# Kernel tuning notes

Measured on AMD Instinct MI355X. Metric: run time of the kernel, lower is better.

Reference implementation:

```python
import jax, jax.numpy as jnp
import numpy as np
from jax import lax

B, DIM, HEADS, H, W = 8, 384, 8, 64, 64
HEAD_C = DIM // HEADS        # 48 -> topk k's: 24, 32, 36, 38
HID = int(DIM * 2.66)        # 1021
EPS_LN = 1e-5
EPS_N = 1e-12
SMALL = 1e-6


def conv2d(x, w, b, pad, groups=1):
    out = lax.conv_general_dilated(
        x, w, (1, 1), [(pad, pad), (pad, pad)],
        feature_group_count=groups,
        dimension_numbers=('NCHW', 'OIHW', 'NCHW'))
    return out + b[None, :, None, None]


def l2n(x):
    # torch F.normalize(dim=-1): x / max(||x||_2, eps)
    n = jnp.linalg.norm(x, axis=-1, keepdims=True)
    return x / jnp.maximum(n, EPS_N)


def layer_norm_c(x, w, b):
    # WithBias LayerNorm over channel dim (module does to_3d -> LN(c) -> to_4d)
    xt = jnp.transpose(x, (0, 2, 3, 1))  # b h w c
    mu = xt.mean(-1, keepdims=True)
    var = xt.var(-1, keepdims=True)      # unbiased=False
    y = (xt - mu) / jnp.sqrt(var + EPS_LN) * w + b
    return jnp.transpose(y, (0, 3, 1, 2))


def setup_inputs() -> dict:
    key = jax.random.key(0)
    ks = iter(jax.random.split(key, 40))
    rn = lambda shape, s=0.02: jax.random.normal(next(ks), shape, jnp.float32) * s
    return dict(
        x=jax.random.normal(next(ks), (B, DIM, H, W), jnp.float32),
        spf=jax.random.normal(next(ks), (1, 3, H, W), jnp.float32),
        ln1_w=jnp.ones((DIM,)), ln1_b=jnp.zeros((DIM,)),
        qkv_w=rn((3 * DIM, DIM, 1, 1)), qkv_b=jnp.zeros((3 * DIM,)),
        qkvdw_w=rn((3 * DIM, 1, 3, 3)), qkvdw_b=jnp.zeros((3 * DIM,)),
        proj_w=rn((DIM, 3, 3, 3)), proj_b=jnp.zeros((DIM,)),
        temperature=jnp.ones((HEADS, 1, 1)),
        a1=jnp.array([0.2]), a2=jnp.array([0.2]),
        a3=jnp.array([0.2]), a4=jnp.array([0.2]),
        wmix=jnp.ones((2,)),
        pout_w=rn((DIM, DIM, 1, 1)), pout_b=jnp.zeros((DIM,)),
        ln2_w=jnp.ones((DIM,)), ln2_b=jnp.zeros((DIM,)),
        pin_w=rn((2 * HID, DIM, 1, 1)), pin_b=jnp.zeros((2 * HID,)),
        dw_w=rn((HID, 1, 3, 3)), dw_b=jnp.zeros((HID,)),
        lin_w=rn((HID, HID)), lin_b=jnp.zeros((HID,)),
        adj_w=rn((HID, 2 * HID, 1, 1)), adj_b=jnp.zeros((HID,)),
        fout_w=rn((DIM, HID, 1, 1)), fout_b=jnp.zeros((DIM,)),
    )


def reference(x, spf, ln1_w, ln1_b, qkv_w, qkv_b, qkvdw_w, qkvdw_b,
              proj_w, proj_b, temperature, a1, a2, a3, a4, wmix,
              pout_w, pout_b, ln2_w, ln2_b, pin_w, pin_b, dw_w, dw_b,
              lin_w, lin_b, adj_w, adj_b, fout_w, fout_b):
    # ---------- Attention ----------
    xn = layer_norm_c(x, ln1_w, ln1_b)
    qkv = conv2d(conv2d(xn, qkv_w, qkv_b, 0), qkvdw_w, qkvdw_b, 1, groups=3 * DIM)
    q, k, v = jnp.split(qkv, 3, axis=1)
    q1 = l2n(q)                               # normalize along W axis
    spm = conv2d(jnp.broadcast_to(l2n(spf), (B, 3, H, W)), proj_w, proj_b, 1)
    qs = l2n((q1 * spm).reshape(B, HEADS, HEAD_C, H * W))
    kr = l2n(k.reshape(B, HEADS, HEAD_C, H * W))
    vr = v.reshape(B, HEADS, HEAD_C, H * W)
    attn = jnp.einsum('bhcn,bhdn->bhcd', qs, kr) * temperature[None]

    def masked_sm(kk):
        thr = lax.top_k(attn, kk)[0][..., -1:]  # k-th largest per row
        return jax.nn.softmax(jnp.where(attn >= thr, attn, attn * SMALL), axis=-1)

    attn0 = jax.nn.relu(attn)
    wsm = jax.nn.softmax(wmix)
    topks = [HEAD_C // 2, 2 * HEAD_C // 3, 3 * HEAD_C // 4, 4 * HEAD_C // 5]
    out = jnp.zeros((B, HEADS, HEAD_C, H * W), attn.dtype)
    for kk, c in zip(topks, [a1, a2, a3, a4]):
        blend = attn0 * wsm[0] + masked_sm(kk) * wsm[1]
        out = out + c * jnp.einsum('bhcd,bhdn->bhcn', blend, vr)
    out = out.reshape(B, DIM, H, W)
    x = x + conv2d(out, pout_w, pout_b, 0)

    # ---------- FeedForward ----------
    xn2 = layer_norm_c(x, ln2_w, ln2_b)
    p = conv2d(xn2, pin_w, pin_b, 0)
    x1, x2 = jnp.split(p, 2, axis=1)
    x1d = conv2d(x1, dw_w, dw_b, 1, groups=HID)
    x2l = jnp.einsum('bchw,oc->bohw', x2, lin_w) + lin_b[None, :, None, None]
    cat = jnp.concatenate([x1d, x2l], axis=1)    # [B, 2*HID, H, W]
    y1 = conv2d(cat, adj_w, adj_b, 0)
    y2 = y1  # second cat is identical under the intended (non-buggy) reading
    f = jax.nn.gelu(y1, approximate=False) * y2
    return x + conv2d(f, fout_w, fout_b, 0)
```

## Files before the change

### kernel.cpp

```cpp
#include <hip/hip_runtime.h>
#include <math.h>

typedef long long i64;
typedef unsigned short u16;
typedef unsigned int u32;

#define DIMC 384
#define DIM3 1152
#define HC 48
#define HWN 4096

using bf16x8 = __attribute__((ext_vector_type(8))) short;
using f32x4 = __attribute__((ext_vector_type(4))) float;

__device__ __forceinline__ float bf2f(u16 u) { u32 x = ((u32)u) << 16; return __uint_as_float(x); }
__device__ __forceinline__ u16 f2bf(float f) {
  u32 u = __float_as_uint(f);
  u32 r = u + 0x7FFFu + ((u >> 16) & 1u);
  return (u16)(r >> 16);
}
__device__ __forceinline__ u16 to_bf16(float f) { return f2bf(f); }
__device__ __forceinline__ u16 to_bf16(u16 u) { return u; }
__device__ __forceinline__ float ld_as_f(const float* p) { return *p; }
__device__ __forceinline__ float ld_as_f(const u16* p) { return bf2f(*p); }

__device__ __forceinline__ void gld_lds16(const u16* g, u16* l) {
  __builtin_amdgcn_global_load_lds(
      (const __attribute__((address_space(1))) void*)g,
      (__attribute__((address_space(3))) void*)l, 16, 0, 0);
}


__global__ void zero_kernel(float* __restrict__ p, int n) {
  int i = blockIdx.x * 256 + threadIdx.x;
  if (i < n) p[i] = 0.f;
}

__global__ void cvt_pad_kernel(const float* __restrict__ src, int lds, int M, int K,
                               u16* __restrict__ out) {
  int idx = blockIdx.x * 256 + threadIdx.x;
  int r = idx >> 10, k = idx & 1023;
  out[idx] = (r < M && k < K) ? f2bf(src[(i64)r * lds + k]) : (u16)0;
}

template <typename T>
__global__ void stats_kernel(const T* __restrict__ x, float* __restrict__ mu,
                             float* __restrict__ rs, int npix4) {
  int idx = blockIdx.x * 256 + threadIdx.x;
  if (idx >= npix4) return;
  int pg = idx * 4;
  int b = pg >> 12, p = pg & 4095;
  const T* xp = x + ((i64)b * DIMC) * HWN + p;
  float s0 = 0.f, s1 = 0.f, s2 = 0.f, s3 = 0.f;
  float q0 = 0.f, q1 = 0.f, q2 = 0.f, q3 = 0.f;
  for (int c = 0; c < DIMC; ++c) {
    const T* rp = xp + (i64)c * HWN;
    float v0 = ld_as_f(rp), v1 = ld_as_f(rp + 1), v2 = ld_as_f(rp + 2), v3 = ld_as_f(rp + 3);
    s0 += v0; s1 += v1; s2 += v2; s3 += v3;
    q0 += v0 * v0; q1 += v1 * v1; q2 += v2 * v2; q3 += v3 * v3;
  }
  const float inv = 1.f / DIMC;
  float4 m = make_float4(s0 * inv, s1 * inv, s2 * inv, s3 * inv);
  float4 r;
  r.x = rsqrtf(q0 * inv - m.x * m.x + 1e-5f);
  r.y = rsqrtf(q1 * inv - m.y * m.y + 1e-5f);
  r.z = rsqrtf(q2 * inv - m.z * m.z + 1e-5f);
  r.w = rsqrtf(q3 * inv - m.w * m.w + 1e-5f);
  *(float4*)(mu + (i64)pg) = m;
  *(float4*)(rs + (i64)pg) = r;
}

template <typename T>
__global__ __launch_bounds__(256) void ln_t_kernel(
    const T* __restrict__ x, const float* __restrict__ mu, const float* __restrict__ rs,
    const float* __restrict__ g, const float* __restrict__ bb, u16* __restrict__ y) {
  __shared__ u16 tile[64][66];
  int p0 = blockIdx.x * 64, c0 = blockIdx.y * 64, b = blockIdx.z;
  int t = threadIdx.x;
  int tp = t & 63, tq = t >> 6;
  float m = mu[b * 4096 + p0 + tp], r = rs[b * 4096 + p0 + tp];
  const T* xp = x + (i64)b * DIMC * HWN + (i64)c0 * 4096 + p0;
#pragma unroll
  for (int i = 0; i < 16; ++i) {
    int c = tq + i * 4;
    float v = ld_as_f(xp + (i64)c * 4096 + tp);
    tile[c][tp] = f2bf((v - m) * r * g[c0 + c] + bb[c0 + c]);
  }
  __syncthreads();
#pragma unroll
  for (int i = 0; i < 16; ++i) {
    int p = tq + i * 4;
    y[((i64)b * 4096 + p0 + p) * 384 + c0 + tp] = tile[tp][p];
  }
}

__global__ __launch_bounds__(256) void dw8_kernel(const u16* __restrict__ in, int ldin,
                                                  const float* __restrict__ w,
                                                  const float* __restrict__ bias,
                                                  u16* __restrict__ out, int ldo, int CH) {
  int t = threadIdx.x;
  int g = t & 31;
  int s = t >> 5;
  int c0 = (blockIdx.y * 32 + g) * 4;
  if (c0 >= ldo) return;
  i64 p0 = (i64)blockIdx.x * 32 + s * 4;
  i64 pb = p0 & ~4095LL;
  int sp = (int)(p0 & 4095);
  int y = sp >> 6, x0 = sp & 63;
  float wv[9][4];
  float acc[4][4];
#pragma unroll
  for (int cc = 0; cc < 4; ++cc) {
    bool val = (c0 + cc) < CH;
    float bv = val ? bias[c0 + cc] : 0.f;
#pragma unroll
    for (int i = 0; i < 4; ++i) acc[i][cc] = bv;
#pragma unroll
    for (int j = 0; j < 9; ++j) wv[j][cc] = val ? w[(c0 + cc) * 9 + j] : 0.f;
  }
#pragma unroll
  for (int dy = 0; dy < 3; ++dy) {
    int yy = y - 1 + dy;
    if ((unsigned)yy >= 64u) continue;
    float row[6][4];
#pragma unroll
    for (int dx = 0; dx < 6; ++dx) {
      int xx = x0 - 1 + dx;
      if ((unsigned)xx < 64u) {
        ushort4 v = *(const ushort4*)(in + (pb + yy * 64 + xx) * ldin + c0);
        row[dx][0] = bf2f(v.x); row[dx][1] = bf2f(v.y);
        row[dx][2] = bf2f(v.z); row[dx][3] = bf2f(v.w);
      } else {
        row[dx][0] = 0.f; row[dx][1] = 0.f; row[dx][2] = 0.f; row[dx][3] = 0.f;
      }
    }
#pragma unroll
    for (int i = 0; i < 4; ++i)
#pragma unroll
      for (int dx = 0; dx < 3; ++dx)
#pragma unroll
        for (int cc = 0; cc < 4; ++cc)
          acc[i][cc] += row[i + dx][cc] * wv[dy * 3 + dx][cc];
  }
#pragma unroll
  for (int i = 0; i < 4; ++i) {
    ushort4 o;
    o.x = (c0 + 0 < CH) ? f2bf(acc[i][0]) : (u16)0;
    o.y = (c0 + 1 < CH) ? f2bf(acc[i][1]) : (u16)0;
    o.z = (c0 + 2 < CH) ? f2bf(acc[i][2]) : (u16)0;
    o.w = (c0 + 3 < CH) ? f2bf(acc[i][3]) : (u16)0;
    *(ushort4*)(out + (p0 + i) * ldo + c0) = o;
  }
}

__global__ __launch_bounds__(192) void dwqnorm_kernel(
    const u16* __restrict__ qkv, const float* __restrict__ w9,
    const float* __restrict__ bias, const float* __restrict__ spm,
    const u16* __restrict__ kv, u16* __restrict__ QS,
    float* __restrict__ qssq, float* __restrict__ kssq) {
  int y = blockIdx.x;
  int b = blockIdx.y;
  int c = blockIdx.z * 192 + threadIdx.x;
  float wv[9];
#pragma unroll
  for (int j = 0; j < 9; ++j) wv[j] = w9[c * 9 + j];
  float bv = bias[c];
  float acc[64];
#pragma unroll
  for (int i = 0; i < 64; ++i) acc[i] = bv;
  i64 rowbase = (i64)b * 4096;
#pragma unroll
  for (int dy = 0; dy < 3; ++dy) {
    int yy = y - 1 + dy;
    if ((unsigned)yy >= 64u) continue;
    const u16* rp = qkv + (rowbase + yy * 64) * 1152 + c;
    float w0 = wv[dy * 3 + 0], w1 = wv[dy * 3 + 1], w2 = wv[dy * 3 + 2];
#pragma unroll
    for (int xi = 0; xi < 64; ++xi) {
      float v = bf2f(rp[(i64)xi * 1152]);
      if (xi > 0) acc[xi - 1] += v * w2;
      acc[xi] += v * w1;
      if (xi < 63) acc[xi + 1] += v * w0;
    }
  }
  float qs = 0.f;
#pragma unroll
  for (int i = 0; i < 64; ++i) qs += acc[i] * acc[i];
  float rw = 1.f / fmaxf(sqrtf(qs), 1e-12f);
  float ps = 0.f;
  const float* sp = spm + (i64)(y * 64) * 384 + c;
  u16* qp = QS + (rowbase + y * 64) * 384 + c;
#pragma unroll
  for (int i = 0; i < 64; ++i) {
    float u = acc[i] * rw * sp[(i64)i * 384];
    qp[(i64)i * 384] = f2bf(u);
    ps += u * u;
  }
  atomicAdd(&qssq[b * 384 + c], ps);
  float ks = 0.f;
  const u16* kp = kv + (rowbase + y * 64) * 768 + c;
#pragma unroll
  for (int i = 0; i < 64; ++i) {
    float kvv = bf2f(kp[(i64)i * 768]);
    ks += kvv * kvv;
  }
  atomicAdd(&kssq[b * 384 + c], ks);
}

__global__ void l2row_kernel(const float* __restrict__ in, float* __restrict__ out) {
  int r = blockIdx.x;
  int lane = threadIdx.x;
  float v = in[r * 64 + lane];
  float ss = v * v;
  for (int o = 32; o > 0; o >>= 1) ss += __shfl_xor(ss, o);
  float n = fmaxf(sqrtf(ss), 1e-12f);
  out[r * 64 + lane] = v / n;
}

__global__ void spm_kernel(const float* __restrict__ s, const float* __restrict__ w,
                           const float* __restrict__ bias, float* __restrict__ out) {
  int idx = blockIdx.x * 256 + threadIdx.x;
  int c = idx % 384, p = idx / 384;
  int xc = p & 63, yr = p >> 6;
  const float* wp = w + c * 27;
  float acc = bias[c];
  for (int ic = 0; ic < 3; ++ic)
    for (int dy = -1; dy <= 1; ++dy) {
      int yy = yr + dy; if ((unsigned)yy >= 64u) continue;
      for (int dx = -1; dx <= 1; ++dx) {
        int xx = xc + dx; if ((unsigned)xx >= 64u) continue;
        acc += s[ic * 4096 + yy * 64 + xx] * wp[ic * 9 + (dy + 1) * 3 + (dx + 1)];
      }
    }
  out[idx] = acc;
}

__global__ __launch_bounds__(256) void attnS_kernel(const u16* __restrict__ QS,
                                                    const u16* __restrict__ kv,
                                                    float* __restrict__ attnP) {
  int ksp = blockIdx.x;
  int bh = blockIdx.y;
  int b = bh >> 3, h = bh & 7;
  __shared__ float qsm[64][49];
  __shared__ float ksm[64][49];
  int t = threadIdx.x, tc = t & 15, td = t >> 4;
  float acc[3][3] = {{0.f}};
  for (int sub = 0; sub < 4; ++sub) {
    i64 nb = (i64)b * 4096 + ksp * 256 + sub * 64;
    __syncthreads();
    for (int l = t; l < 4096; l += 256) {
      int row = l >> 6, cq = l & 63;
      if (cq < 48) {
        qsm[row][cq] = bf2f(QS[(nb + row) * 384 + h * 48 + cq]);
        ksm[row][cq] = bf2f(kv[(nb + row) * 768 + h * 48 + cq]);
      }
    }
    __syncthreads();
#pragma unroll 4
    for (int nn = 0; nn < 64; ++nn) {
      float a0 = qsm[nn][tc], a1 = qsm[nn][tc + 16], a2 = qsm[nn][tc + 32];
      float b0 = ksm[nn][td], b1 = ksm[nn][td + 16], b2 = ksm[nn][td + 32];
      acc[0][0] += a0 * b0; acc[0][1] += a0 * b1; acc[0][2] += a0 * b2;
      acc[1][0] += a1 * b0; acc[1][1] += a1 * b1; acc[1][2] += a1 * b2;
      acc[2][0] += a2 * b0; acc[2][1] += a2 * b1; acc[2][2] += a2 * b2;
    }
  }
  float* ap = attnP + ((i64)bh * 16 + ksp) * 2304;
#pragma unroll
  for (int i = 0; i < 3; ++i)
#pragma unroll
    for (int j = 0; j < 3; ++j)
      ap[(tc + 16 * i) * HC + (td + 16 * j)] = acc[i][j];
}

__global__ void blend_kernel(const float* __restrict__ attnP, const float* __restrict__ qssq,
                             const float* __restrict__ kssq, const float* __restrict__ temp,
                             const float* __restrict__ wmix, const float* __restrict__ pa1,
                             const float* __restrict__ pa2, const float* __restrict__ pa3,
                             const float* __restrict__ pa4, float* __restrict__ comb) {
  int row = blockIdx.x * 4 + (threadIdx.x >> 6);
  int lane = threadIdx.x & 63;
  int bh = row / 48, cc = row - bh * 48;
  int b = bh >> 3, h = bh & 7;
  float a;
  if (lane < 48) {
    const float* pp = attnP + ((i64)bh * 16) * 2304 + cc * 48 + lane;
    float s = 0.f;
#pragma unroll
    for (int sp = 0; sp < 16; ++sp) s += pp[(i64)sp * 2304];
    float qn = 1.f / fmaxf(sqrtf(qssq[b * 384 + h * 48 + cc]), 1e-12f);
    float kn = 1.f / fmaxf(sqrtf(kssq[b * 384 + h * 48 + lane]), 1e-12f);
    a = s * qn * kn * temp[h];
  } else {
    a = -INFINITY;
  }
  int rank = 0;
  for (int j = 0; j < 48; ++j) {
    float aj = __shfl(a, j);
    rank += (aj > a) ? 1 : 0;
  }
  float w0 = wmix[0], w1 = wmix[1];
  float wm = fmaxf(w0, w1);
  float e0 = expf(w0 - wm), e1 = expf(w1 - wm);
  float ws0 = e0 / (e0 + e1), ws1 = e1 / (e0 + e1);
  float c1 = pa1[0], c2 = pa2[0], c3 = pa3[0], c4 = pa4[0];
  float outv = ws0 * (c1 + c2 + c3 + c4) * fmaxf(a, 0.f);
  const int kks[4] = {24, 32, 36, 38};
  const float cs[4] = {c1, c2, c3, c4};
#pragma unroll
  for (int q = 0; q < 4; ++q) {
    float mv = (lane < 48) ? ((rank < kks[q]) ? a : a * 1e-6f) : -INFINITY;
    float mx = mv;
    for (int o = 32; o > 0; o >>= 1) mx = fmaxf(mx, __shfl_xor(mx, o));
    float e = (lane < 48) ? expf(mv - mx) : 0.f;
    float s = e;
    for (int o = 32; o > 0; o >>= 1) s += __shfl_xor(s, o);
    outv += ws1 * cs[q] * (e / s);
  }
  if (lane < 48) comb[(i64)row * 48 + lane] = outv;
}

__global__ __launch_bounds__(384) void combv_kernel(const u16* __restrict__ kv,
                                                    const float* __restrict__ comb,
                                                    u16* __restrict__ AO) {
  __shared__ float Vs[4][8][49];
  i64 p0 = (i64)blockIdx.x * 4;
  int b = (int)(p0 >> 12);
  int t = threadIdx.x;
  int h = t / 48, cc = t - h * 48;
#pragma unroll
  for (int px = 0; px < 4; ++px)
    Vs[px][h][cc] = bf2f(kv[(p0 + px) * 768 + 384 + t]);
  __syncthreads();
  float cr[48];
  const float* cp = comb + ((i64)(b * 8 + h) * 48 + cc) * 48;
#pragma unroll
  for (int d = 0; d < 48; d += 4) {
    float4 v = *(const float4*)(cp + d);
    cr[d] = v.x; cr[d + 1] = v.y; cr[d + 2] = v.z; cr[d + 3] = v.w;
  }
#pragma unroll
  for (int px = 0; px < 4; ++px) {
    float s = 0.f;
#pragma unroll
    for (int d = 0; d < 48; ++d) s += cr[d] * Vs[px][h][d];
    AO[(p0 + px) * 384 + t] = f2bf(s);
  }
}

__global__ void matvec_kernel(const float* __restrict__ Wm, int ldw, int koff,
                              const float* __restrict__ v, const float* __restrict__ add,
                              float* __restrict__ out, int K) {
  int ro = blockIdx.x;
  int t = threadIdx.x;
  const float* wp = Wm + (i64)ro * ldw + koff;
  float s = 0.f;
  for (int k = t; k < K; k += 256) s += wp[k] * v[k];
  __shared__ float sred[256];
  sred[t] = s;
  __syncthreads();
  for (int o = 128; o > 0; o >>= 1) {
    if (t < o) sred[t] += sred[t + o];
    __syncthreads();
  }
  if (t == 0) out[ro] = sred[0] + (add ? add[ro] : 0.f);
}

template <typename T>
__global__ void pack_w_kernel(const T* __restrict__ W, int ldw, int koff, int M, int K,
                              int KS, u16* __restrict__ out, int nfrag) {
  int tid = blockIdx.x * 256 + threadIdx.x;
  int lane = tid & 63;
  int idx = tid >> 6;
  if (idx >= nfrag * KS) return;
  int ks = idx % KS, fm = idx / KS;
  int row = fm * 16 + (lane & 15);
  int kb = ks * 32 + (lane >> 4) * 8;
  union { u16 us[8]; uint4 q; } u;
#pragma unroll
  for (int j = 0; j < 8; ++j) {
    int k = kb + j;
    u.us[j] = (row < M && k < K) ? to_bf16(W[(i64)row * ldw + koff + k]) : (u16)0;
  }
  *(uint4*)(out + (i64)idx * 512 + lane * 8) = u.q;
}

template <typename T>
__global__ void pack_wT_kernel(const T* __restrict__ src, int ldk, i64 kbase, int M, int K,
                               int KS, u16* __restrict__ out, int nfrag) {
  int tid = blockIdx.x * 256 + threadIdx.x;
  int lane = tid & 63;
  int idx = tid >> 6;
  if (idx >= nfrag * KS) return;
  int ks = idx % KS, fm = idx / KS;
  int row = fm * 16 + (lane & 15);
  int kb = ks * 32 + (lane >> 4) * 8;
  union { u16 us[8]; uint4 q; } u;
#pragma unroll
  for (int j = 0; j < 8; ++j) {
    int k = kb + j;
    u.us[j] = (row < M && k < K) ? to_bf16(src[(kbase + k) * (i64)ldk + row]) : (u16)0;
  }
  *(uint4*)(out + (i64)idx * 512 + lane * 8) = u.q;
}

template <int NF>
__global__ __launch_bounds__(NF * 32) void gemm_nk_kernel(
    const u16* __restrict__ A1, int lda1, int KS1, const u16* __restrict__ Wp1,
    const u16* __restrict__ A2, int lda2, int KS2, const u16* __restrict__ Wp2,
    int nfrag, const float* __restrict__ bias,
    const void* __restrict__ Res, float* __restrict__ Yf, u16* __restrict__ Yh,
    int ldo, int M, int epi) {
  __shared__ __align__(16) u16 Ls[2][NF + 8][512];
  int t = threadIdx.x, lane = t & 63, w = t >> 6;
  int wn = w >> 1, wm = w & 1;
  i64 n0 = (i64)blockIdx.x * (NF * 16);
  int mt = blockIdx.y;

  f32x4 acc[4][4];
#pragma unroll
  for (int i = 0; i < 4; ++i)
#pragma unroll
    for (int r = 0; r < 4; ++r) acc[i][r] = (f32x4){0.f, 0.f, 0.f, 0.f};

  auto stage = [&](int kt, int buf) {
    const u16* A; int lda; const u16* Wp; int KSc; int ks;
    if (kt < KS1) { A = A1; lda = lda1; Wp = Wp1; KSc = KS1; ks = kt; }
    else { A = A2; lda = lda2; Wp = Wp2; KSc = KS2; ks = kt - KS1; }
#pragma unroll
    for (int j = 0; j < 2; ++j) {
      int f = w * 2 + j;
      const u16* srcA = A + (n0 + f * 16 + (lane & 15)) * (i64)lda + ks * 32 + (lane >> 4) * 8;
      gld_lds16(srcA, &Ls[buf][f][0]);
    }
    if constexpr (NF == 8) {
#pragma unroll
      for (int j = 0; j < 2; ++j) {
        int f = w * 2 + j;
        int fmc = min(mt * 8 + f, nfrag - 1);
        gld_lds16(Wp + ((i64)fmc * KSc + ks) * 512 + lane * 8, &Ls[buf][NF + f][0]);
      }
    } else {
      int fmc = min(mt * 8 + w, nfrag - 1);
      gld_lds16(Wp + ((i64)fmc * KSc + ks) * 512 + lane * 8, &Ls[buf][NF + w][0]);
    }
  };

  int KT = KS1 + KS2;
  stage(0, 0);
  __syncthreads();
  int s = 0;
  for (int kt = 0; kt < KT; ++kt) {
    if (kt + 1 < KT) stage(kt + 1, s ^ 1);
    bf16x8 af[4], wf[4];
#pragma unroll
    for (int i = 0; i < 4; ++i) {
      af[i] = *reinterpret_cast<const bf16x8*>(&Ls[s][wn * 4 + i][lane * 8]);
      wf[i] = *reinterpret_cast<const bf16x8*>(&Ls[s][NF + wm * 4 + i][lane * 8]);
    }
#pragma unroll
    for (int i = 0; i < 4; ++i)
#pragma unroll
      for (int r = 0; r < 4; ++r)
        acc[i][r] = __builtin_amdgcn_mfma_f32_16x16x32_bf16(af[i], wf[r], acc[i][r], 0, 0, 0);
    __syncthreads();
    s ^= 1;
  }

#pragma unroll
  for (int i = 0; i < 4; ++i) {
    int nbase = (int)n0 + (wn * 4 + i) * 16 + ((lane >> 4) << 2);
#pragma unroll
    for (int r = 0; r < 4; ++r) {
      int m = mt * 128 + (wm * 4 + r) * 16 + (lane & 15);
      if (epi == 1 || epi == 3) {
        if (m < M) {
          float bv = bias[m];
          int b = nbase >> 12, p = nbase & 4095;
          i64 off = ((i64)b * DIMC + m) * 4096 + p;
          if (epi == 1) {
            float4 rv = *(const float4*)((const float*)Res + off);
            ushort4 o;
            o.x = f2bf(acc[i][r][0] + bv + rv.x);
            o.y = f2bf(acc[i][r][1] + bv + rv.y);
            o.z = f2bf(acc[i][r][2] + bv + rv.z);
            o.w = f2bf(acc[i][r][3] + bv + rv.w);
            *(ushort4*)(Yh + off) = o;
          } else {
            ushort4 rv = *(const ushort4*)((const u16*)Res + off);
            float4 o;
            o.x = acc[i][r][0] + bv + bf2f(rv.x);
            o.y = acc[i][r][1] + bv + bf2f(rv.y);
            o.z = acc[i][r][2] + bv + bf2f(rv.z);
            o.w = acc[i][r][3] + bv + bf2f(rv.w);
            *(float4*)(Yf + off) = o;
          }
        }
      } else {
        if (m < ldo) {
          float bv = (m < M) ? bias[m] : 0.f;
#pragma unroll
          for (int ii = 0; ii < 4; ++ii) {
            float v = acc[i][r][ii] + bv;
            if (epi == 2) {
              float gg = 0.5f * v * (1.f + erff(v * 0.70710678118f));
              v = gg * v;
            }
            if (m >= M) v = 0.f;
            Yh[(i64)(nbase + ii) * ldo + m] = f2bf(v);
          }
        }
      }
    }
  }
}


extern "C" void kernel_launch(void* const* d_in, const int* in_sizes, int n_in,
                              void* d_out, int out_size, void* d_ws, size_t ws_size,
                              hipStream_t stream) {
  (void)in_sizes; (void)n_in; (void)out_size;
  const float* x       = (const float*)d_in[0];
  const float* spf     = (const float*)d_in[1];
  const float* ln1_w   = (const float*)d_in[2];
  const float* ln1_b   = (const float*)d_in[3];
  const float* qkv_w   = (const float*)d_in[4];
  const float* qkv_b   = (const float*)d_in[5];
  const float* qkvdw_w = (const float*)d_in[6];
  const float* qkvdw_b = (const float*)d_in[7];
  const float* proj_w  = (const float*)d_in[8];
  const float* proj_b  = (const float*)d_in[9];
  const float* temp    = (const float*)d_in[10];
  const float* a1      = (const float*)d_in[11];
  const float* a2      = (const float*)d_in[12];
  const float* a3      = (const float*)d_in[13];
  const float* a4      = (const float*)d_in[14];
  const float* wmix    = (const float*)d_in[15];
  const float* pout_w  = (const float*)d_in[16];
  const float* pout_b  = (const float*)d_in[17];
  const float* ln2_w   = (const float*)d_in[18];
  const float* ln2_b   = (const float*)d_in[19];
  const float* pin_w   = (const float*)d_in[20];
  const float* pin_b   = (const float*)d_in[21];
  const float* dw_w    = (const float*)d_in[22];
  const float* dw_b    = (const float*)d_in[23];
  const float* lin_w   = (const float*)d_in[24];
  const float* lin_b   = (const float*)d_in[25];
  const float* adj_w   = (const float*)d_in[26];
  const float* adj_b   = (const float*)d_in[27];
  const float* fout_w  = (const float*)d_in[28];
  const float* fout_b  = (const float*)d_in[29];
  float* out = (float*)d_out;
  float* ws = (float*)d_ws;

  const i64 PLANE = (i64)DIMC * HWN;
  const i64 FIXED = 4543488;
  const i64 PER = 6342656;
  int C = 8;
  while (C > 1 && (size_t)(FIXED + PER * C) * 4 > ws_size) C >>= 1;
  if ((size_t)(FIXED + PER * C) * 4 > ws_size) return;
  int nch = 8 / C;

  float* SPM   = ws;
  float* b2v   = SPM + 1572864;
  float* b3v   = b2v + 1024;
  float* zbias = b3v + 1024;
  float* spfn  = zbias + 1024;
  float* mu1   = spfn + 12288;
  float* rs1   = mu1 + 32768;
  float* mu2   = rs1 + 32768;
  float* rs2   = mu2 + 32768;
  float* qssq  = rs2 + 32768;
  float* kssq  = qssq + 3072;
  float* packbase = kssq + 3072;
  u16* qkv_wp  = (u16*)packbase;
  u16* pout_wp = qkv_wp + 884736;
  u16* pin_wp  = pout_wp + 294912;
  u16* adj1_wp = pin_wp + 786432;
  u16* W3_wp   = adj1_wp + 2097152;
  u16* fout_wp = W3_wp + 786432;
  float* dyn   = packbase + 2818048;

  float* attnP = dyn;
  float* comb  = attnP + (i64)C * 294912;
  float* RA    = comb + (i64)C * 18432;
  float* RD    = RA + (i64)C * 786432;
  float* RB    = RD + (i64)C * 786432;
  float* RC    = RB + (i64)C * 2359296;

  u16* linbf    = (u16*)dyn;
  u16* adjbf    = linbf + 1048576;
  u16* W2bf     = adjbf + 1048576;
  u16* W3bf     = W2bf + 393216;
  u16* pin2T_wp = W3bf + 393216;
  u16* W2T_wp   = pin2T_wp + 393216;

  zero_kernel<<<dim3(4), dim3(256), 0, stream>>>(zbias, 1024);
  matvec_kernel<<<dim3(1021), dim3(256), 0, stream>>>(lin_w, 1021, 0, pin_b + 1021, lin_b, b2v, 1021);
  matvec_kernel<<<dim3(1021), dim3(256), 0, stream>>>(adj_w, 2042, 1021, b2v, adj_b, b3v, 1021);
  cvt_pad_kernel<<<dim3(4096), dim3(256), 0, stream>>>(lin_w, 1021, 1021, 1021, linbf);
  cvt_pad_kernel<<<dim3(4096), dim3(256), 0, stream>>>(adj_w + 1021, 2042, 1021, 1021, adjbf);
  pack_wT_kernel<float><<<dim3(192), dim3(256), 0, stream>>>(pin_w, 384, 1021, 384, 1021, 32,
                                                             pin2T_wp, 24);
  gemm_nk_kernel<8><<<dim3(8, 3), dim3(256), 0, stream>>>(
      linbf, 1024, 32, pin2T_wp, nullptr, 0, 0, nullptr, 24,
      zbias, nullptr, nullptr, W2bf, 384, 384, 0);
  pack_wT_kernel<u16><<<dim3(192), dim3(256), 0, stream>>>(W2bf, 384, 0, 384, 1021, 32,
                                                           W2T_wp, 24);
  gemm_nk_kernel<8><<<dim3(8, 3), dim3(256), 0, stream>>>(
      adjbf, 1024, 32, W2T_wp, nullptr, 0, 0, nullptr, 24,
      zbias, nullptr, nullptr, W3bf, 384, 384, 0);
  pack_w_kernel<u16><<<dim3(192), dim3(256), 0, stream>>>(W3bf, 384, 0, 1021, 384, 12, W3_wp, 64);

  pack_w_kernel<float><<<dim3(216), dim3(256), 0, stream>>>(qkv_w, 384, 0, 1152, 384, 12, qkv_wp, 72);
  pack_w_kernel<float><<<dim3(72), dim3(256), 0, stream>>>(pout_w, 384, 0, 384, 384, 12, pout_wp, 24);
  pack_w_kernel<float><<<dim3(192), dim3(256), 0, stream>>>(pin_w, 384, 0, 1021, 384, 12, pin_wp, 64);
  pack_w_kernel<float><<<dim3(512), dim3(256), 0, stream>>>(adj_w, 2042, 0, 1021, 1021, 32, adj1_wp, 64);
  pack_w_kernel<float><<<dim3(192), dim3(256), 0, stream>>>(fout_w, 1021, 0, 384, 1021, 32, fout_wp, 24);

  l2row_kernel<<<dim3(192), dim3(64), 0, stream>>>(spf, spfn);
  spm_kernel<<<dim3(6144), dim3(256), 0, stream>>>(spfn, proj_w, proj_b, SPM);
  stats_kernel<float><<<dim3(32), dim3(256), 0, stream>>>(x, mu1, rs1, 8192);

  for (int ch = 0; ch < nch; ++ch) {
    int b0 = ch * C;
    const float* xb = x + (i64)b0 * PLANE;
    float* outb = out + (i64)b0 * PLANE;
    const float* m1 = mu1 + (i64)b0 * HWN;
    const float* r1 = rs1 + (i64)b0 * HWN;

    u16* Xbf    = (u16*)RA;
    u16* qkv_bf = (u16*)RB;
    u16* kvb    = (u16*)RC;
    u16* QS     = (u16*)RA;
    u16* AO     = (u16*)RA;
    u16* xatt   = (u16*)RD;
    u16* xn2    = (u16*)RA;
    u16* x1     = (u16*)RB;
    u16* x1d    = (u16*)RC;
    u16* fbf    = (u16*)RB;

    int NB16 = C * 16;
    int NB8  = C * 32;

    zero_kernel<<<dim3((2 * C * 384 + 255) / 256), dim3(256), 0, stream>>>(qssq, 2 * C * 384);
    ln_t_kernel<float><<<dim3(64, 6, C), dim3(256), 0, stream>>>(xb, m1, r1, ln1_w, ln1_b, Xbf);
    gemm_nk_kernel<16><<<dim3(NB16, 9), dim3(512), 0, stream>>>(
        Xbf, 384, 12, qkv_wp, nullptr, 0, 0, nullptr, 72,
        qkv_b, nullptr, nullptr, qkv_bf, 1152, 1152, 0);
    dw8_kernel<<<dim3(C * 128, 6), dim3(256), 0, stream>>>(
        qkv_bf + 384, 1152, qkvdw_w + 384 * 9, qkvdw_b + 384, kvb, 768, 768);
    dwqnorm_kernel<<<dim3(64, C, 2), dim3(192), 0, stream>>>(
        qkv_bf, qkvdw_w, qkvdw_b, SPM, kvb, QS, qssq, kssq);
    attnS_kernel<<<dim3(16, C * 8), dim3(256), 0, stream>>>(QS, kvb, attnP);
    blend_kernel<<<dim3(96 * C), dim3(256), 0, stream>>>(attnP, qssq, kssq, temp, wmix,
                                                         a1, a2, a3, a4, comb);
    combv_kernel<<<dim3(C * 1024), dim3(384), 0, stream>>>(kvb, comb, AO);
    gemm_nk_kernel<8><<<dim3(NB8, 3), dim3(256), 0, stream>>>(
        AO, 384, 12, pout_wp, nullptr, 0, 0, nullptr, 24,
        pout_b, xb, nullptr, xatt, 0, 384, 1);

    stats_kernel<u16><<<dim3((C * 1024 + 255) / 256), dim3(256), 0, stream>>>(xatt, mu2, rs2,
                                                                              C * 1024);
    ln_t_kernel<u16><<<dim3(64, 6, C), dim3(256), 0, stream>>>(xatt, mu2, rs2, ln2_w, ln2_b, xn2);
    gemm_nk_kernel<16><<<dim3(NB16, 8), dim3(512), 0, stream>>>(
        xn2, 384, 12, pin_wp, nullptr, 0, 0, nullptr, 64,
        pin_b, nullptr, nullptr, x1, 1024, 1021, 0);
    dw8_kernel<<<dim3(C * 128, 8), dim3(256), 0, stream>>>(
        x1, 1024, dw_w, dw_b, x1d, 1024, 1021);
    gemm_nk_kernel<16><<<dim3(NB16, 8), dim3(512), 0, stream>>>(
        x1d, 1024, 32, adj1_wp, xn2, 384, 12, W3_wp, 64,
        b3v, nullptr, nullptr, fbf, 1024, 1021, 2);
    gemm_nk_kernel<8><<<dim3(NB8, 3), dim3(256), 0, stream>>>(
        fbf, 1024, 32, fout_wp, nullptr, 0, 0, nullptr, 24,
        fout_b, xatt, outb, nullptr, 0, 384, 3);
  }
}
```

Measured before the change: 928.4 us.

## Swap MFMA operands for vectorized NHWC epilogue stores and split q/kv outputs

```diff
diff --git a/kernel.cpp b/kernel.cpp
--- a/kernel.cpp
+++ b/kernel.cpp
@@ -30,11 +30,6 @@
       (__attribute__((address_space(3))) void*)l, 16, 0, 0);
 }
 
-
-__global__ void zero_kernel(float* __restrict__ p, int n) {
-  int i = blockIdx.x * 256 + threadIdx.x;
-  if (i < n) p[i] = 0.f;
-}
 
 __global__ void cvt_pad_kernel(const float* __restrict__ src, int lds, int M, int K,
                                u16* __restrict__ out) {
@@ -154,7 +149,7 @@
 }
 
 __global__ __launch_bounds__(192) void dwqnorm_kernel(
-    const u16* __restrict__ qkv, const float* __restrict__ w9,
+    const u16* __restrict__ qraw, const float* __restrict__ w9,
     const float* __restrict__ bias, const float* __restrict__ spm,
     const u16* __restrict__ kv, u16* __restrict__ QS,
     float* __restrict__ qssq, float* __restrict__ kssq) {
@@ -173,11 +168,11 @@
   for (int dy = 0; dy < 3; ++dy) {
     int yy = y - 1 + dy;
     if ((unsigned)yy >= 64u) continue;
-    const u16* rp = qkv + (rowbase + yy * 64) * 1152 + c;
+    const u16* rp = qraw + (rowbase + yy * 64) * 384 + c;
     float w0 = wv[dy * 3 + 0], w1 = wv[dy * 3 + 1], w2 = wv[dy * 3 + 2];
 #pragma unroll
     for (int xi = 0; xi < 64; ++xi) {
-      float v = bf2f(rp[(i64)xi * 1152]);
+      float v = bf2f(rp[(i64)xi * 384]);
       if (xi > 0) acc[xi - 1] += v * w2;
       acc[xi] += v * w1;
       if (xi < 63) acc[xi + 1] += v * w0;
@@ -404,13 +399,14 @@
   *(uint4*)(out + (i64)idx * 512 + lane * 8) = u.q;
 }
 
-template <int NF>
+template <int NF, bool SWAP>
 __global__ __launch_bounds__(NF * 32) void gemm_nk_kernel(
     const u16* __restrict__ A1, int lda1, int KS1, const u16* __restrict__ Wp1,
     const u16* __restrict__ A2, int lda2, int KS2, const u16* __restrict__ Wp2,
     int nfrag, const float* __restrict__ bias,
     const void* __restrict__ Res, float* __restrict__ Yf, u16* __restrict__ Yh,
-    int ldo, int M, int epi) {
+    int ldo, int msplit, u16* __restrict__ Yh2, int ld2,
+    int M, int epi) {
   __shared__ __align__(16) u16 Ls[2][NF + 8][512];
   int t = threadIdx.x, lane = t & 63, w = t >> 6;
   int wn = w >> 1, wm = w & 1;
@@ -461,19 +457,49 @@
 #pragma unroll
     for (int i = 0; i < 4; ++i)
 #pragma unroll
-      for (int r = 0; r < 4; ++r)
-        acc[i][r] = __builtin_amdgcn_mfma_f32_16x16x32_bf16(af[i], wf[r], acc[i][r], 0, 0, 0);
+      for (int r = 0; r < 4; ++r) {
+        if constexpr (SWAP)
+          acc[i][r] = __builtin_amdgcn_mfma_f32_16x16x32_bf16(wf[r], af[i], acc[i][r], 0, 0, 0);
+        else
+          acc[i][r] = __builtin_amdgcn_mfma_f32_16x16x32_bf16(af[i], wf[r], acc[i][r], 0, 0, 0);
+      }
     __syncthreads();
     s ^= 1;
   }
 
-#pragma unroll
-  for (int i = 0; i < 4; ++i) {
-    int nbase = (int)n0 + (wn * 4 + i) * 16 + ((lane >> 4) << 2);
-#pragma unroll
-    for (int r = 0; r < 4; ++r) {
-      int m = mt * 128 + (wm * 4 + r) * 16 + (lane & 15);
-      if (epi == 1 || epi == 3) {
+  if constexpr (SWAP) {
+#pragma unroll
+    for (int i = 0; i < 4; ++i) {
+      i64 n = n0 + (wn * 4 + i) * 16 + (lane & 15);
+#pragma unroll
+      for (int r = 0; r < 4; ++r) {
+        int m4 = mt * 128 + (wm * 4 + r) * 16 + ((lane >> 4) << 2);
+        float4 bv = *(const float4*)(bias + m4);
+        float v0 = acc[i][r][0] + bv.x;
+        float v1 = acc[i][r][1] + bv.y;
+        float v2 = acc[i][r][2] + bv.z;
+        float v3 = acc[i][r][3] + bv.w;
+        if (epi == 2) {
+          float g0 = 0.5f * v0 * (1.f + erff(v0 * 0.70710678118f));
+          float g1 = 0.5f * v1 * (1.f + erff(v1 * 0.70710678118f));
+          float g2 = 0.5f * v2 * (1.f + erff(v2 * 0.70710678118f));
+          float g3 = 0.5f * v3 * (1.f + erff(v3 * 0.70710678118f));
+          v0 *= g0; v1 *= g1; v2 *= g2; v3 *= g3;
+        }
+        ushort4 o;
+        o.x = f2bf(v0); o.y = f2bf(v1); o.z = f2bf(v2); o.w = f2bf(v3);
+        u16* dst = (m4 < msplit) ? (Yh + n * (i64)ldo + m4)
+                                 : (Yh2 + n * (i64)ld2 + (m4 - msplit));
+        *(ushort4*)dst = o;
+      }
+    }
+  } else {
+#pragma unroll
+    for (int i = 0; i < 4; ++i) {
+      int nbase = (int)n0 + (wn * 4 + i) * 16 + ((lane >> 4) << 2);
+#pragma unroll
+      for (int r = 0; r < 4; ++r) {
+        int m = mt * 128 + (wm * 4 + r) * 16 + (lane & 15);
         if (m < M) {
           float bv = bias[m];
           int b = nbase >> 12, p = nbase & 4095;
@@ -494,20 +520,6 @@
             o.z = acc[i][r][2] + bv + bf2f(rv.z);
             o.w = acc[i][r][3] + bv + bf2f(rv.w);
             *(float4*)(Yf + off) = o;
-          }
-        }
-      } else {
-        if (m < ldo) {
-          float bv = (m < M) ? bias[m] : 0.f;
-#pragma unroll
-          for (int ii = 0; ii < 4; ++ii) {
-            float v = acc[i][r][ii] + bv;
-            if (epi == 2) {
-              float gg = 0.5f * v * (1.f + erff(v * 0.70710678118f));
-              v = gg * v;
-            }
-            if (m >= M) v = 0.f;
-            Yh[(i64)(nbase + ii) * ldo + m] = f2bf(v);
           }
         }
       }
@@ -595,21 +607,21 @@
   u16* pin2T_wp = W3bf + 393216;
   u16* W2T_wp   = pin2T_wp + 393216;
 
-  zero_kernel<<<dim3(4), dim3(256), 0, stream>>>(zbias, 1024);
+  hipMemsetAsync(b2v, 0, 3 * 1024 * sizeof(float), stream);
   matvec_kernel<<<dim3(1021), dim3(256), 0, stream>>>(lin_w, 1021, 0, pin_b + 1021, lin_b, b2v, 1021);
   matvec_kernel<<<dim3(1021), dim3(256), 0, stream>>>(adj_w, 2042, 1021, b2v, adj_b, b3v, 1021);
   cvt_pad_kernel<<<dim3(4096), dim3(256), 0, stream>>>(lin_w, 1021, 1021, 1021, linbf);
   cvt_pad_kernel<<<dim3(4096), dim3(256), 0, stream>>>(adj_w + 1021, 2042, 1021, 1021, adjbf);
   pack_wT_kernel<float><<<dim3(192), dim3(256), 0, stream>>>(pin_w, 384, 1021, 384, 1021, 32,
                                                              pin2T_wp, 24);
-  gemm_nk_kernel<8><<<dim3(8, 3), dim3(256), 0, stream>>>(
+  gemm_nk_kernel<8, true><<<dim3(8, 3), dim3(256), 0, stream>>>(
       linbf, 1024, 32, pin2T_wp, nullptr, 0, 0, nullptr, 24,
-      zbias, nullptr, nullptr, W2bf, 384, 384, 0);
+      zbias, nullptr, nullptr, W2bf, 384, 1 << 30, nullptr, 0, 384, 0);
   pack_wT_kernel<u16><<<dim3(192), dim3(256), 0, stream>>>(W2bf, 384, 0, 384, 1021, 32,
                                                            W2T_wp, 24);
-  gemm_nk_kernel<8><<<dim3(8, 3), dim3(256), 0, stream>>>(
+  gemm_nk_kernel<8, true><<<dim3(8, 3), dim3(256), 0, stream>>>(
       adjbf, 1024, 32, W2T_wp, nullptr, 0, 0, nullptr, 24,
-      zbias, nullptr, nullptr, W3bf, 384, 384, 0);
+      zbias, nullptr, nullptr, W3bf, 384, 1 << 30, nullptr, 0, 384, 0);
   pack_w_kernel<u16><<<dim3(192), dim3(256), 0, stream>>>(W3bf, 384, 0, 1021, 384, 12, W3_wp, 64);
 
   pack_w_kernel<float><<<dim3(216), dim3(256), 0, stream>>>(qkv_w, 384, 0, 1152, 384, 12, qkv_wp, 72);
@@ -629,50 +641,51 @@
     const float* m1 = mu1 + (i64)b0 * HWN;
     const float* r1 = rs1 + (i64)b0 * HWN;
 
-    u16* Xbf    = (u16*)RA;
-    u16* qkv_bf = (u16*)RB;
-    u16* kvb    = (u16*)RC;
-    u16* QS     = (u16*)RA;
-    u16* AO     = (u16*)RA;
-    u16* xatt   = (u16*)RD;
-    u16* xn2    = (u16*)RA;
-    u16* x1     = (u16*)RB;
-    u16* x1d    = (u16*)RC;
-    u16* fbf    = (u16*)RB;
+    i64 NTOT = (i64)C * 4096;
+    u16* Xbf   = (u16*)RA;
+    u16* qraw  = (u16*)RB;
+    u16* kvraw = qraw + NTOT * 384;
+    u16* kvb   = (u16*)RC;
+    u16* QS    = (u16*)RA;
+    u16* AO    = (u16*)RA;
+    u16* xatt  = (u16*)RD;
+    u16* xn2   = (u16*)RA;
+    u16* x1    = (u16*)RB;
+    u16* x1d   = (u16*)RC;
+    u16* fbf   = (u16*)RB;
 
     int NB16 = C * 16;
-    int NB8  = C * 32;
-
-    zero_kernel<<<dim3((2 * C * 384 + 255) / 256), dim3(256), 0, stream>>>(qssq, 2 * C * 384);
+
+    hipMemsetAsync(qssq, 0, 2 * 3072 * sizeof(float), stream);
     ln_t_kernel<float><<<dim3(64, 6, C), dim3(256), 0, stream>>>(xb, m1, r1, ln1_w, ln1_b, Xbf);
-    gemm_nk_kernel<16><<<dim3(NB16, 9), dim3(512), 0, stream>>>(
+    gemm_nk_kernel<16, true><<<dim3(NB16, 9), dim3(512), 0, stream>>>(
         Xbf, 384, 12, qkv_wp, nullptr, 0, 0, nullptr, 72,
-        qkv_b, nullptr, nullptr, qkv_bf, 1152, 1152, 0);
+        qkv_b, nullptr, nullptr, qraw, 384, 384, kvraw, 768, 1152, 0);
     dw8_kernel<<<dim3(C * 128, 6), dim3(256), 0, stream>>>(
-        qkv_bf + 384, 1152, qkvdw_w + 384 * 9, qkvdw_b + 384, kvb, 768, 768);
+        kvraw, 768, qkvdw_w + 384 * 9, qkvdw_b + 384, kvb, 768, 768);
     dwqnorm_kernel<<<dim3(64, C, 2), dim3(192), 0, stream>>>(
-        qkv_bf, qkvdw_w, qkvdw_b, SPM, kvb, QS, qssq, kssq);
+        qraw, qkvdw_w, qkvdw_b, SPM, kvb, QS, qssq, kssq);
     attnS_kernel<<<dim3(16, C * 8), dim3(256), 0, stream>>>(QS, kvb, attnP);
     blend_kernel<<<dim3(96 * C), dim3(256), 0, stream>>>(attnP, qssq, kssq, temp, wmix,
                                                          a1, a2, a3, a4, comb);
     combv_kernel<<<dim3(C * 1024), dim3(384), 0, stream>>>(kvb, comb, AO);
-    gemm_nk_kernel<8><<<dim3(NB8, 3), dim3(256), 0, stream>>>(
+    gemm_nk_kernel<16, false><<<dim3(NB16, 3), dim3(512), 0, stream>>>(
         AO, 384, 12, pout_wp, nullptr, 0, 0, nullptr, 24,
-        pout_b, xb, nullptr, xatt, 0, 384, 1);
+        pout_b, xb, nullptr, xatt, 0, 1 << 30, nullptr, 0, 384, 1);
 
     stats_kernel<u16><<<dim3((C * 1024 + 255) / 256), dim3(256), 0, stream>>>(xatt, mu2, rs2,
                                                                               C * 1024);
     ln_t_kernel<u16><<<dim3(64, 6, C), dim3(256), 0, stream>>>(xatt, mu2, rs2, ln2_w, ln2_b, xn2);
-    gemm_nk_kernel<16><<<dim3(NB16, 8), dim3(512), 0, stream>>>(
+    gemm_nk_kernel<16, true><<<dim3(NB16, 8), dim3(512), 0, stream>>>(
         xn2, 384, 12, pin_wp, nullptr, 0, 0, nullptr, 64,
-        pin_b, nullptr, nullptr, x1, 1024, 1021, 0);
+        pin_b, nullptr, nullptr, x1, 1024, 1 << 30, nullptr, 0, 1021, 0);
     dw8_kernel<<<dim3(C * 128, 8), dim3(256), 0, stream>>>(
         x1, 1024, dw_w, dw_b, x1d, 1024, 1021);
-    gemm_nk_kernel<16><<<dim3(NB16, 8), dim3(512), 0, stream>>>(
+    gemm_nk_kernel<16, true><<<dim3(NB16, 8), dim3(512), 0, stream>>>(
         x1d, 1024, 32, adj1_wp, xn2, 384, 12, W3_wp, 64,
-        b3v, nullptr, nullptr, fbf, 1024, 1021, 2);
-    gemm_nk_kernel<8><<<dim3(NB8, 3), dim3(256), 0, stream>>>(
+        b3v, nullptr, nullptr, fbf, 1024, 1 << 30, nullptr, 0, 1021, 2);
+    gemm_nk_kernel<16, false><<<dim3(NB16, 3), dim3(512), 0, stream>>>(
         fbf, 1024, 32, fout_wp, nullptr, 0, 0, nullptr, 24,
-        fout_b, xatt, outb, nullptr, 0, 384, 3);
-  }
-}
+        fout_b, xatt, outb, nullptr, 0, 1 << 30, nullptr, 0, 384, 3);
+  }
+}
```

After: 895.4 us. 3.6% less time.
